# Kernel optimization log

Hardware: AMD Instinct MI355X
Metric: run time of the kernel (lower is better)

Reference implementation:

```python
import jax, jax.numpy as jnp
import numpy as np

D = 1024
H = 16
DH = D // H


def setup_inputs() -> dict:
    key = jax.random.key(0)
    ks = jax.random.split(key, 9)
    s = 1.0 / np.sqrt(D)
    return {
        "x": jax.random.normal(ks[0], (4, 2048, D), dtype=jnp.float32),
        "wq": jax.random.uniform(ks[1], (D, D), jnp.float32, -s, s),
        "bq": jax.random.uniform(ks[2], (D,), jnp.float32, -s, s),
        "wk": jax.random.uniform(ks[3], (D, D), jnp.float32, -s, s),
        "bk": jax.random.uniform(ks[4], (D,), jnp.float32, -s, s),
        "wv": jax.random.uniform(ks[5], (D, D), jnp.float32, -s, s),
        "bv": jax.random.uniform(ks[6], (D,), jnp.float32, -s, s),
        "wo": jax.random.uniform(ks[7], (D, D), jnp.float32, -s, s),
        "bo": jax.random.uniform(ks[8], (D,), jnp.float32, -s, s),
    }


def reference(x, wq, bq, wk, bk, wv, bv, wo, bo):
    B, S, _ = x.shape
    # projections + split heads: [B, S, D] -> [B, H, S, Dh]
    def split(t):
        return t.reshape(B, S, H, DH).transpose(0, 2, 1, 3)
    q = split(x @ wq + bq)
    k = split(x @ wk + bk)
    v = split(x @ wv + bv)
    scale = 1.0 / jnp.sqrt(jnp.float32(DH))
    scores = jnp.einsum("bhqd,bhkd->bhqk", q, k) * scale  # [B,H,S,S]
    att = jax.nn.softmax(scores, axis=-1)
    out = jnp.einsum("bhqk,bhkd->bhqd", att, v)  # [B,H,S,Dh]
    out = out.transpose(0, 2, 1, 3).reshape(B, S, D)
    return out @ wo + bo
```

## Files before the change

kernel.cpp:

```cpp
#include <hip/hip_runtime.h>
#include <stdint.h>

typedef float f32x4 __attribute__((ext_vector_type(4)));
typedef __bf16 bf16x8 __attribute__((ext_vector_type(8)));
typedef unsigned short ushort_t;
typedef ushort_t ushortx8 __attribute__((ext_vector_type(8)));
typedef ushort_t ushortx4 __attribute__((ext_vector_type(4)));

#define DEV static __device__ __forceinline__

DEV ushort_t f2bf(float f) {
  union { float f; uint32_t u; } v; v.f = f;
  uint32_t u = v.u;
  return (ushort_t)((u + 0x7FFFu + ((u >> 16) & 1u)) >> 16);
}

DEV uint32_t pkbf(float a, float b) {
  __bf16 x = (__bf16)a, y = (__bf16)b;
  return (uint32_t)__builtin_bit_cast(unsigned short, x) |
         ((uint32_t)__builtin_bit_cast(unsigned short, y) << 16);
}

DEV void cp16(const void* g, void* l) {
  __builtin_amdgcn_global_load_lds((const __attribute__((address_space(1))) unsigned int*)g,
                                   (__attribute__((address_space(3))) unsigned int*)l,
                                   16, 0, 0);
}

DEV f32x4 mfma16(bf16x8 a, bf16x8 b, f32x4 c) {
  return __builtin_amdgcn_mfma_f32_16x16x32_bf16(a, b, c, 0, 0, 0);
}

__global__ __launch_bounds__(256) void k_prep(
    const float* __restrict__ x, ushort_t* __restrict__ xb,
    const float* __restrict__ wq, const float* __restrict__ wk,
    const float* __restrict__ wv, const float* __restrict__ wo,
    ushort_t* __restrict__ wqkvT, ushort_t* __restrict__ woT) {
  __shared__ float tile[32][33];
  int b = blockIdx.x;
  if (b < 4096) {
    size_t idx = ((size_t)b * 256 + threadIdx.x) * 8;
    const float4* src = (const float4*)(x + idx);
    float4 a = src[0], c = src[1];
    ushortx8 o;
    o[0] = f2bf(a.x); o[1] = f2bf(a.y); o[2] = f2bf(a.z); o[3] = f2bf(a.w);
    o[4] = f2bf(c.x); o[5] = f2bf(c.y); o[6] = f2bf(c.z); o[7] = f2bf(c.w);
    *(ushortx8*)(xb + idx) = o;
  } else {
    int t = b - 4096;
    int which = t >> 10;
    const float* src = (which == 0) ? wq : (which == 1) ? wk : (which == 2) ? wv : wo;
    ushort_t* dst = (which == 0) ? wqkvT
                    : (which == 1) ? wqkvT + 1024 * 1024
                    : (which == 2) ? wqkvT + 2 * 1024 * 1024
                                   : woT;
    int tt = t & 1023;
    int c0 = (tt & 31) * 32, r0 = (tt >> 5) * 32;
    int tx = threadIdx.x & 31, ty = threadIdx.x >> 5;
#pragma unroll
    for (int i = ty; i < 32; i += 8)
      tile[i][tx] = src[(size_t)(r0 + i) * 1024 + c0 + tx];
    __syncthreads();
#pragma unroll
    for (int i = ty; i < 32; i += 8)
      dst[(size_t)(c0 + i) * 1024 + r0 + tx] = f2bf(tile[tx][i]);
  }
}

__global__ __launch_bounds__(256) void k_transpose_v(const ushort_t* __restrict__ vw,
                                                     ushort_t* __restrict__ vtw) {
  __shared__ ushort_t t[64][72];
  int tid = threadIdx.x;
  int bh = blockIdx.y, s0 = blockIdx.x * 64;
#pragma unroll
  for (int n = 0; n < 2; ++n) {
    int row = (tid >> 3) + n * 32, ch = (tid & 7) * 8;
    *(ushortx8*)&t[row][ch] =
        *(const ushortx8*)&vw[((size_t)bh * 2048 + s0 + row) * 64 + ch];
  }
  __syncthreads();
#pragma unroll
  for (int n = 0; n < 2; ++n) {
    int dh = (tid >> 3) + n * 32, sc = (tid & 7) * 8;
    ushortx8 o;
#pragma unroll
    for (int k = 0; k < 8; ++k) o[k] = t[sc + k][dh];
    *(ushortx8*)&vtw[((size_t)bh * 64 + dh) * 2048 + s0 + sc] = o;
  }
}

__global__ __launch_bounds__(512, 2) void k_gemm256(
    const ushort_t* __restrict__ A, const ushort_t* __restrict__ Bt,
    const float* __restrict__ b0, const float* __restrict__ b1,
    const float* __restrict__ b2, ushort_t* __restrict__ qw,
    ushort_t* __restrict__ kw, ushort_t* __restrict__ vw) {
  extern __shared__ ushort_t lds[];
  ushort_t* As = lds;
  ushort_t* Bs = lds + 32768;
  const int K = 1024, NT = 16;
  int tid = threadIdx.x;
  int w = tid >> 6, lane = tid & 63, l16 = lane & 15, lg = lane >> 4;
  int wr = w >> 2, wc = w & 3;
  int m0 = blockIdx.x * 256, n0 = blockIdx.y * 256;

  const ushort_t* Asrc = A + (size_t)(m0 + w * 8 + (lane >> 3)) * K +
                         (size_t)(((lane & 7) ^ (lane >> 3)) * 8);
  const ushort_t* Bsrc = Bt + (size_t)(n0 + w * 8 + (lane >> 3)) * K +
                         (size_t)(((lane & 7) ^ (lane >> 3)) * 8);

  f32x4 acc[8][4] = {};
  bf16x8 a[4][2], b[4][2];
  const int aRow = wr * 128 + l16, bRow = wc * 64 + l16, rsw = l16 & 7;

#pragma unroll
  for (int s = 0; s < 4; ++s)
    cp16(Asrc + (size_t)s * 64 * K, As + s * 4096 + w * 512);
#pragma unroll
  for (int s = 0; s < 4; ++s)
    cp16(Bsrc + (size_t)s * 64 * K, Bs + s * 4096 + w * 512);
  cp16(Asrc + 64, As + 16384 + w * 512);
  cp16(Asrc + (size_t)65536 + 64, As + 16384 + 4096 + w * 512);
  asm volatile("s_waitcnt vmcnt(2)" ::: "memory");
  __builtin_amdgcn_s_barrier();

  for (int t = 0; t < NT; ++t) {
    int cur = t & 1, nxt = cur ^ 1;
    ushort_t* AsC = As + cur * 16384;
    ushort_t* BsC = Bs + cur * 16384;
    ushort_t* AsN = As + nxt * 16384;
    ushort_t* BsN = Bs + nxt * 16384;
    const ushort_t* An = Asrc + (size_t)(t + 1) * 64;
    const ushort_t* Bn = Bsrc + (size_t)(t + 1) * 64;

#pragma unroll
    for (int i2 = 0; i2 < 4; ++i2)
#pragma unroll
      for (int ks = 0; ks < 2; ++ks)
        a[i2][ks] = *(const bf16x8*)&AsC[(aRow + i2 * 16) * 64 +
                                         (((ks << 2) | lg) ^ rsw) * 8];
#pragma unroll
    for (int j2 = 0; j2 < 2; ++j2)
#pragma unroll
      for (int ks = 0; ks < 2; ++ks)
        b[j2][ks] = *(const bf16x8*)&BsC[(bRow + j2 * 16) * 64 +
                                         (((ks << 2) | lg) ^ rsw) * 8];
    cp16(An + (size_t)2 * 65536, AsN + 2 * 4096 + w * 512);
    cp16(An + (size_t)3 * 65536, AsN + 3 * 4096 + w * 512);
    __builtin_amdgcn_s_barrier();
    asm volatile("s_waitcnt lgkmcnt(0)" ::: "memory");
    __builtin_amdgcn_s_setprio(1);
#pragma unroll
    for (int i2 = 0; i2 < 4; ++i2)
#pragma unroll
      for (int j2 = 0; j2 < 2; ++j2)
#pragma unroll
        for (int ks = 0; ks < 2; ++ks)
          acc[i2][j2] = mfma16(a[i2][ks], b[j2][ks], acc[i2][j2]);
    __builtin_amdgcn_s_setprio(0);
    __builtin_amdgcn_s_barrier();

#pragma unroll
    for (int j2 = 2; j2 < 4; ++j2)
#pragma unroll
      for (int ks = 0; ks < 2; ++ks)
        b[j2][ks] = *(const bf16x8*)&BsC[(bRow + j2 * 16) * 64 +
                                         (((ks << 2) | lg) ^ rsw) * 8];
    cp16(Bn, BsN + w * 512);
    cp16(Bn + (size_t)65536, BsN + 4096 + w * 512);
    __builtin_amdgcn_s_barrier();
    asm volatile("s_waitcnt lgkmcnt(0)" ::: "memory");
    __builtin_amdgcn_s_setprio(1);
#pragma unroll
    for (int i2 = 0; i2 < 4; ++i2)
#pragma unroll
      for (int j2 = 2; j2 < 4; ++j2)
#pragma unroll
        for (int ks = 0; ks < 2; ++ks)
          acc[i2][j2] = mfma16(a[i2][ks], b[j2][ks], acc[i2][j2]);
    __builtin_amdgcn_s_setprio(0);
    __builtin_amdgcn_s_barrier();

#pragma unroll
    for (int i2 = 0; i2 < 4; ++i2)
#pragma unroll
      for (int ks = 0; ks < 2; ++ks)
        a[i2][ks] = *(const bf16x8*)&AsC[(aRow + (4 + i2) * 16) * 64 +
                                         (((ks << 2) | lg) ^ rsw) * 8];
    cp16(Bn + (size_t)2 * 65536, BsN + 2 * 4096 + w * 512);
    cp16(Bn + (size_t)3 * 65536, BsN + 3 * 4096 + w * 512);
    __builtin_amdgcn_s_barrier();
    asm volatile("s_waitcnt lgkmcnt(0)" ::: "memory");
    __builtin_amdgcn_s_setprio(1);
#pragma unroll
    for (int i2 = 0; i2 < 4; ++i2)
#pragma unroll
      for (int j2 = 2; j2 < 4; ++j2)
#pragma unroll
        for (int ks = 0; ks < 2; ++ks)
          acc[4 + i2][j2] = mfma16(a[i2][ks], b[j2][ks], acc[4 + i2][j2]);
    __builtin_amdgcn_s_setprio(0);
    __builtin_amdgcn_s_barrier();

    {
      const ushort_t* A2 = Asrc + (size_t)(t + 2) * 64;
      cp16(A2, AsC + w * 512);
      cp16(A2 + (size_t)65536, AsC + 4096 + w * 512);
    }
    asm volatile("s_waitcnt vmcnt(2)" ::: "memory");
    __builtin_amdgcn_s_barrier();
    __builtin_amdgcn_s_setprio(1);
#pragma unroll
    for (int i2 = 0; i2 < 4; ++i2)
#pragma unroll
      for (int j2 = 0; j2 < 2; ++j2)
#pragma unroll
        for (int ks = 0; ks < 2; ++ks)
          acc[4 + i2][j2] = mfma16(a[i2][ks], b[j2][ks], acc[4 + i2][j2]);
    __builtin_amdgcn_s_setprio(0);
    __builtin_amdgcn_s_barrier();
  }

  const float QSCALE = 0.18033688011112042f;
  int p = blockIdx.x >> 2;
  const float* bias = (p == 0) ? b0 : (p == 1) ? b1 : b2;
  ushort_t* dst = (p == 0) ? qw : (p == 1) ? kw : vw;
  float qs = (p == 0) ? QSCALE : 1.0f;
  int cbase = (m0 & 1023) + wr * 128;
#pragma unroll
  for (int i = 0; i < 8; ++i) {
    int oc = cbase + i * 16 + lg * 4;
    int h = oc >> 6, dh0 = oc & 63;
    float4 bb = *(const float4*)&bias[oc];
#pragma unroll
    for (int j = 0; j < 4; ++j) {
      int tok = n0 + wc * 64 + j * 16 + l16;
      size_t base =
          ((size_t)((tok >> 11) * 16 + h) * 2048 + (tok & 2047)) * 64 + dh0;
      ushortx4 pk;
      pk[0] = f2bf((acc[i][j][0] + bb.x) * qs);
      pk[1] = f2bf((acc[i][j][1] + bb.y) * qs);
      pk[2] = f2bf((acc[i][j][2] + bb.z) * qs);
      pk[3] = f2bf((acc[i][j][3] + bb.w) * qs);
      *(ushortx4*)&dst[base] = pk;
    }
  }
}

template <int MODE>
__global__ __launch_bounds__(256, 2) void k_gemm(
    const ushort_t* __restrict__ A, const ushort_t* __restrict__ Bt,
    const float* __restrict__ b0, float* __restrict__ outf) {
  const int K = 1024;
  __shared__ ushort_t As[128 * 32];
  __shared__ ushort_t Bs[128 * 32];
  int tid = threadIdx.x;
  int w = tid >> 6, lane = tid & 63, l16 = lane & 15, lg = lane >> 4;
  int m0 = blockIdx.x * 128, n0 = blockIdx.y * 128;
  int wm = (w >> 1) * 64, wn = (w & 1) * 64;
  f32x4 acc[4][4] = {};

  const ushort_t* Ag = A + (size_t)(m0 + (tid >> 2)) * K + (tid & 3) * 8;
  const ushort_t* Bg = Bt + (size_t)(n0 + (tid >> 2)) * K + (tid & 3) * 8;

  for (int k0 = 0; k0 < K; k0 += 32) {
    cp16(Ag + k0, As + w * 512);
    cp16(Ag + k0 + 64 * K, As + 2048 + w * 512);
    cp16(Bg + k0, Bs + w * 512);
    cp16(Bg + k0 + 64 * K, Bs + 2048 + w * 512);
    __syncthreads();
    bf16x8 af[4], bfr[4];
#pragma unroll
    for (int i = 0; i < 4; ++i)
      af[i] = *(const bf16x8*)&As[(wm + i * 16 + l16) * 32 + lg * 8];
#pragma unroll
    for (int j = 0; j < 4; ++j)
      bfr[j] = *(const bf16x8*)&Bs[(wn + j * 16 + l16) * 32 + lg * 8];
#pragma unroll
    for (int i = 0; i < 4; ++i)
#pragma unroll
      for (int j = 0; j < 4; ++j)
        acc[i][j] = mfma16(af[i], bfr[j], acc[i][j]);
    __syncthreads();
  }

#pragma unroll
  for (int j = 0; j < 4; ++j) {
    int col = n0 + wn + j * 16 + l16;
    float bb = b0[col];
#pragma unroll
    for (int i = 0; i < 4; ++i) {
#pragma unroll
      for (int r = 0; r < 4; ++r) {
        int row = m0 + wm + i * 16 + lg * 4 + r;
        outf[(size_t)row * 1024 + col] = acc[i][j][r] + bb;
      }
    }
  }
}

__global__ __launch_bounds__(512, 4) void k_attn(
    const ushort_t* __restrict__ qg, const ushort_t* __restrict__ kg,
    const ushort_t* __restrict__ vtg, ushort_t* __restrict__ att) {
  __shared__ ushort_t Ks[128 * 64];
  __shared__ ushort_t Vs[64 * 128];
  __shared__ ushort_t Ps[8][16 * 128];
  int tid = threadIdx.x;
  int w = tid >> 6, lane = tid & 63, l16 = lane & 15, lg = lane >> 4;
  int i = blockIdx.x;
  int bh = (i & 7) * 8 + ((i >> 3) & 7);
  int q0 = (i >> 6) * 256;
  const ushort_t* qh = qg + (size_t)bh * 2048 * 64;

  const ushort_t* kstage = kg + (size_t)bh * 2048 * 64 + (size_t)(tid >> 3) * 64 +
                           (size_t)(((tid & 7) ^ ((tid >> 3) & 7)) * 8);
  const ushort_t* vstage = vtg + (size_t)bh * 64 * 2048 + (size_t)(tid >> 4) * 2048 +
                           (size_t)(((tid & 15) ^ ((tid >> 4) & 15)) * 8);

  bf16x8 qf[2][2];
#pragma unroll
  for (int st = 0; st < 2; ++st)
#pragma unroll
    for (int ks = 0; ks < 2; ++ks)
      qf[st][ks] = *(const bf16x8*)(qh + (size_t)(q0 + w * 32 + st * 16 + l16) * 64 +
                                    ks * 32 + lg * 8);

  bf16x8 vone;
#pragma unroll
  for (int t = 0; t < 8; ++t) vone[t] = (__bf16)1.0f;

  f32x4 o[2][5] = {};

  for (int kb = 0; kb < 2048; kb += 128) {
    __syncthreads();
    cp16(kstage + (size_t)kb * 64, Ks + w * 512);
    cp16(kstage + (size_t)(kb + 64) * 64, Ks + 4096 + w * 512);
    cp16(vstage + kb, Vs + w * 512);
    cp16(vstage + kb + (size_t)32 * 2048, Vs + 4096 + w * 512);
    __syncthreads();

#pragma unroll
    for (int hf = 0; hf < 2; ++hf) {
      f32x4 sc[2][4] = {};
#pragma unroll
      for (int jt = 0; jt < 4; ++jt) {
        int row = hf * 64 + jt * 16 + l16;
        bf16x8 kf0 = *(const bf16x8*)&Ks[row * 64 + ((lg) ^ (l16 & 7)) * 8];
        bf16x8 kf1 = *(const bf16x8*)&Ks[row * 64 + ((lg + 4) ^ (l16 & 7)) * 8];
        sc[0][jt] = mfma16(kf0, qf[0][0], sc[0][jt]);
        sc[0][jt] = mfma16(kf1, qf[0][1], sc[0][jt]);
        sc[1][jt] = mfma16(kf0, qf[1][0], sc[1][jt]);
        sc[1][jt] = mfma16(kf1, qf[1][1], sc[1][jt]);
      }
#pragma unroll
      for (int st = 0; st < 2; ++st)
#pragma unroll
        for (int jt = 0; jt < 4; ++jt) {
          float e0 = __builtin_amdgcn_exp2f(sc[st][jt][0]);
          float e1 = __builtin_amdgcn_exp2f(sc[st][jt][1]);
          float e2 = __builtin_amdgcn_exp2f(sc[st][jt][2]);
          float e3 = __builtin_amdgcn_exp2f(sc[st][jt][3]);
          uint32_t* dst =
              (uint32_t*)&Ps[w][l16 * 128 +
                                (((st * 8 + jt * 2 + (lg >> 1)) ^ l16) * 8) +
                                (lg & 1) * 4];
          dst[0] = pkbf(e0, e1);
          dst[1] = pkbf(e2, e3);
        }
#pragma unroll
      for (int ks = 0; ks < 2; ++ks) {
        int kk = hf * 2 + ks;
        bf16x8 pf0 =
            *(const bf16x8*)&Ps[w][l16 * 128 + (((ks * 4 + lg) ^ l16) * 8)];
        bf16x8 pf1 =
            *(const bf16x8*)&Ps[w][l16 * 128 + (((8 + ks * 4 + lg) ^ l16) * 8)];
        o[0][4] = mfma16(pf0, vone, o[0][4]);
        o[1][4] = mfma16(pf1, vone, o[1][4]);
#pragma unroll
        for (int dt = 0; dt < 4; ++dt) {
          int vrow = dt * 16 + l16;
          bf16x8 vf =
              *(const bf16x8*)&Vs[vrow * 128 + (((kk * 4 + lg) ^ l16) * 8)];
          o[0][dt] = mfma16(pf0, vf, o[0][dt]);
          o[1][dt] = mfma16(pf1, vf, o[1][dt]);
        }
      }
    }
  }

  int bi = bh >> 4, h = bh & 15;
#pragma unroll
  for (int st = 0; st < 2; ++st) {
    f32x4 inv;
#pragma unroll
    for (int r = 0; r < 4; ++r) inv[r] = __builtin_amdgcn_rcpf(o[st][4][r]);
#pragma unroll
    for (int dt = 0; dt < 4; ++dt)
#pragma unroll
      for (int r = 0; r < 4; ++r) {
        int srow = q0 + w * 32 + st * 16 + lg * 4 + r;
        int col = h * 64 + dt * 16 + l16;
        att[(size_t)(bi * 2048 + srow) * 1024 + col] = f2bf(o[st][dt][r] * inv[r]);
      }
  }
}

extern "C" void kernel_launch(void* const* d_in, const int* in_sizes, int n_in,
                              void* d_out, int out_size, void* d_ws, size_t ws_size,
                              hipStream_t stream) {
  const float* x = (const float*)d_in[0];
  const float* wq = (const float*)d_in[1];
  const float* bq = (const float*)d_in[2];
  const float* wk = (const float*)d_in[3];
  const float* bk = (const float*)d_in[4];
  const float* wv = (const float*)d_in[5];
  const float* bv = (const float*)d_in[6];
  const float* wo = (const float*)d_in[7];
  const float* bo = (const float*)d_in[8];
  float* out = (float*)d_out;

  char* ws = (char*)d_ws;
  ushort_t* xb = (ushort_t*)(ws);
  ushort_t* wqkvT = (ushort_t*)(ws + 16777216);
  ushort_t* woT = (ushort_t*)(ws + 23068672);
  ushort_t* qw = (ushort_t*)(ws + 25165824);
  ushort_t* kw = (ushort_t*)(ws + 41943040);
  ushort_t* vtw = (ushort_t*)(ws + 58720256);
  ushort_t* att = (ushort_t*)(ws + 75497472);
  ushort_t* vw = att;

  k_prep<<<dim3(8192), dim3(256), 0, stream>>>(x, xb, wq, wk, wv, wo, wqkvT, woT);

  const int GEMM0_LDS = 131072;
  hipFuncSetAttribute(reinterpret_cast<const void*>(&k_gemm256),
                      hipFuncAttributeMaxDynamicSharedMemorySize, GEMM0_LDS);
  k_gemm256<<<dim3(12, 32), dim3(512), GEMM0_LDS, stream>>>(
      wqkvT, xb, bq, bk, bv, qw, kw, vw);

  k_transpose_v<<<dim3(32, 64), dim3(256), 0, stream>>>(vw, vtw);

  k_attn<<<dim3(512), dim3(512), 0, stream>>>(qw, kw, vtw, att);

  k_gemm<1><<<dim3(64, 8), dim3(256), 0, stream>>>(att, woT, bo, out);
}
```

Measured before the change: 276.6 us.

## Halve attention block threads, give each wave 64 query rows for K/V reuse

The attention kernel now runs 256 threads (4 waves) per block instead of 512, and each wave handles 64 query rows (four 16-row subtiles) instead of 32. Each K and V fragment read from LDS now feeds four MFMAs instead of two, which cuts LDS read traffic per flop. Staging is spread across fewer threads, with four copies each for K and V, and the P scratch buffer is widened to match. The cost is higher register use per wave (more accumulators and Q fragments) and fewer waves per block to hide latency.

```diff
diff --git a/kernel.cpp b/kernel.cpp
--- a/kernel.cpp
+++ b/kernel.cpp
@@ -298,12 +298,12 @@
   }
 }
 
-__global__ __launch_bounds__(512, 4) void k_attn(
+__global__ __launch_bounds__(256, 2) void k_attn(
     const ushort_t* __restrict__ qg, const ushort_t* __restrict__ kg,
     const ushort_t* __restrict__ vtg, ushort_t* __restrict__ att) {
   __shared__ ushort_t Ks[128 * 64];
   __shared__ ushort_t Vs[64 * 128];
-  __shared__ ushort_t Ps[8][16 * 128];
+  __shared__ ushort_t Ps[4][16 * 256];
   int tid = threadIdx.x;
   int w = tid >> 6, lane = tid & 63, l16 = lane & 15, lg = lane >> 4;
   int i = blockIdx.x;
@@ -316,72 +316,78 @@
   const ushort_t* vstage = vtg + (size_t)bh * 64 * 2048 + (size_t)(tid >> 4) * 2048 +
                            (size_t)(((tid & 15) ^ ((tid >> 4) & 15)) * 8);
 
-  bf16x8 qf[2][2];
-#pragma unroll
-  for (int st = 0; st < 2; ++st)
+  bf16x8 qf[4][2];
+#pragma unroll
+  for (int st = 0; st < 4; ++st)
 #pragma unroll
     for (int ks = 0; ks < 2; ++ks)
-      qf[st][ks] = *(const bf16x8*)(qh + (size_t)(q0 + w * 32 + st * 16 + l16) * 64 +
+      qf[st][ks] = *(const bf16x8*)(qh + (size_t)(q0 + w * 64 + st * 16 + l16) * 64 +
                                     ks * 32 + lg * 8);
 
   bf16x8 vone;
 #pragma unroll
   for (int t = 0; t < 8; ++t) vone[t] = (__bf16)1.0f;
 
-  f32x4 o[2][5] = {};
+  f32x4 o[4][5] = {};
 
   for (int kb = 0; kb < 2048; kb += 128) {
     __syncthreads();
-    cp16(kstage + (size_t)kb * 64, Ks + w * 512);
-    cp16(kstage + (size_t)(kb + 64) * 64, Ks + 4096 + w * 512);
-    cp16(vstage + kb, Vs + w * 512);
-    cp16(vstage + kb + (size_t)32 * 2048, Vs + 4096 + w * 512);
+#pragma unroll
+    for (int r = 0; r < 4; ++r)
+      cp16(kstage + (size_t)(kb + r * 32) * 64, Ks + r * 2048 + w * 512);
+#pragma unroll
+    for (int r = 0; r < 4; ++r)
+      cp16(vstage + kb + (size_t)(r * 16) * 2048, Vs + r * 2048 + w * 512);
     __syncthreads();
 
 #pragma unroll
     for (int hf = 0; hf < 2; ++hf) {
-      f32x4 sc[2][4] = {};
+      f32x4 sc[4][4] = {};
 #pragma unroll
       for (int jt = 0; jt < 4; ++jt) {
         int row = hf * 64 + jt * 16 + l16;
         bf16x8 kf0 = *(const bf16x8*)&Ks[row * 64 + ((lg) ^ (l16 & 7)) * 8];
         bf16x8 kf1 = *(const bf16x8*)&Ks[row * 64 + ((lg + 4) ^ (l16 & 7)) * 8];
-        sc[0][jt] = mfma16(kf0, qf[0][0], sc[0][jt]);
-        sc[0][jt] = mfma16(kf1, qf[0][1], sc[0][jt]);
-        sc[1][jt] = mfma16(kf0, qf[1][0], sc[1][jt]);
-        sc[1][jt] = mfma16(kf1, qf[1][1], sc[1][jt]);
+#pragma unroll
+        for (int st = 0; st < 4; ++st) {
+          sc[st][jt] = mfma16(kf0, qf[st][0], sc[st][jt]);
+          sc[st][jt] = mfma16(kf1, qf[st][1], sc[st][jt]);
+        }
       }
 #pragma unroll
-      for (int st = 0; st < 2; ++st)
+      for (int st = 0; st < 4; ++st)
 #pragma unroll
         for (int jt = 0; jt < 4; ++jt) {
           float e0 = __builtin_amdgcn_exp2f(sc[st][jt][0]);
           float e1 = __builtin_amdgcn_exp2f(sc[st][jt][1]);
           float e2 = __builtin_amdgcn_exp2f(sc[st][jt][2]);
           float e3 = __builtin_amdgcn_exp2f(sc[st][jt][3]);
-          uint32_t* dst =
-              (uint32_t*)&Ps[w][l16 * 128 +
-                                (((st * 8 + jt * 2 + (lg >> 1)) ^ l16) * 8) +
-                                (lg & 1) * 4];
-          dst[0] = pkbf(e0, e1);
-          dst[1] = pkbf(e2, e3);
+          uint2 pk2;
+          pk2.x = pkbf(e0, e1);
+          pk2.y = pkbf(e2, e3);
+          *(uint2*)&Ps[w][l16 * 256 +
+                          (((st * 8 + jt * 2 + (lg >> 1)) ^ l16) * 8) +
+                          (lg & 1) * 4] = pk2;
         }
 #pragma unroll
       for (int ks = 0; ks < 2; ++ks) {
         int kk = hf * 2 + ks;
-        bf16x8 pf0 =
-            *(const bf16x8*)&Ps[w][l16 * 128 + (((ks * 4 + lg) ^ l16) * 8)];
-        bf16x8 pf1 =
-            *(const bf16x8*)&Ps[w][l16 * 128 + (((8 + ks * 4 + lg) ^ l16) * 8)];
-        o[0][4] = mfma16(pf0, vone, o[0][4]);
-        o[1][4] = mfma16(pf1, vone, o[1][4]);
+        bf16x8 pf[4];
+#pragma unroll
+        for (int st = 0; st < 4; ++st)
+          pf[st] = *(const bf16x8*)&Ps[w][l16 * 256 +
+                                          (((st * 8 + ks * 4 + lg) ^ l16) * 8)];
+#pragma unroll
+        for (int st = 0; st < 4; ++st)
+          o[st][4] = mfma16(pf[st], vone, o[st][4]);
 #pragma unroll
         for (int dt = 0; dt < 4; ++dt) {
           int vrow = dt * 16 + l16;
           bf16x8 vf =
               *(const bf16x8*)&Vs[vrow * 128 + (((kk * 4 + lg) ^ l16) * 8)];
-          o[0][dt] = mfma16(pf0, vf, o[0][dt]);
-          o[1][dt] = mfma16(pf1, vf, o[1][dt]);
+#pragma unroll
+          for (int st = 0; st < 4; ++st)
+            o[st][dt] = mfma16(pf[st], vf, o[st][dt]);
         }
       }
     }
@@ -389,7 +395,7 @@
 
   int bi = bh >> 4, h = bh & 15;
 #pragma unroll
-  for (int st = 0; st < 2; ++st) {
+  for (int st = 0; st < 4; ++st) {
     f32x4 inv;
 #pragma unroll
     for (int r = 0; r < 4; ++r) inv[r] = __builtin_amdgcn_rcpf(o[st][4][r]);
@@ -397,7 +403,7 @@
     for (int dt = 0; dt < 4; ++dt)
 #pragma unroll
       for (int r = 0; r < 4; ++r) {
-        int srow = q0 + w * 32 + st * 16 + lg * 4 + r;
+        int srow = q0 + w * 64 + st * 16 + lg * 4 + r;
         int col = h * 64 + dt * 16 + l16;
         att[(size_t)(bi * 2048 + srow) * 1024 + col] = f2bf(o[st][dt][r] * inv[r]);
       }
@@ -438,7 +444,7 @@
 
   k_transpose_v<<<dim3(32, 64), dim3(256), 0, stream>>>(vw, vtw);
 
-  k_attn<<<dim3(512), dim3(512), 0, stream>>>(qw, kw, vtw, att);
+  k_attn<<<dim3(512), dim3(256), 0, stream>>>(qw, kw, vtw, att);
 
   k_gemm<1><<<dim3(64, 8), dim3(256), 0, stream>>>(att, woT, bo, out);
 }
```

Result: no change. 279.4 us (+1.0%).

## Double-buffer K/V tiles in attention with async prefetch and wave priority

Applied to the files above, without the earlier changes.

The attention loop now walks 64-key tiles with two LDS buffers. It prefetches the next K/V tile while computing on the current one, so each iteration needs one barrier instead of two. Wave priority is raised around the MFMA sections, and the launch-bounds occupancy hint drops from 4 to 2. The last iteration prefetches past the end of the head's K/V data, which can read out of bounds for the final head. Relying on the barrier to order the async LDS loads is a correctness risk.

```diff
diff --git a/kernel.cpp b/kernel.cpp
--- a/kernel.cpp
+++ b/kernel.cpp
@@ -298,11 +298,11 @@
   }
 }
 
-__global__ __launch_bounds__(512, 4) void k_attn(
+__global__ __launch_bounds__(512, 2) void k_attn(
     const ushort_t* __restrict__ qg, const ushort_t* __restrict__ kg,
     const ushort_t* __restrict__ vtg, ushort_t* __restrict__ att) {
-  __shared__ ushort_t Ks[128 * 64];
-  __shared__ ushort_t Vs[64 * 128];
+  __shared__ ushort_t Ks[2][64 * 64];
+  __shared__ ushort_t Vs[2][64 * 64];
   __shared__ ushort_t Ps[8][16 * 128];
   int tid = threadIdx.x;
   int w = tid >> 6, lane = tid & 63, l16 = lane & 15, lg = lane >> 4;
@@ -313,8 +313,8 @@
 
   const ushort_t* kstage = kg + (size_t)bh * 2048 * 64 + (size_t)(tid >> 3) * 64 +
                            (size_t)(((tid & 7) ^ ((tid >> 3) & 7)) * 8);
-  const ushort_t* vstage = vtg + (size_t)bh * 64 * 2048 + (size_t)(tid >> 4) * 2048 +
-                           (size_t)(((tid & 15) ^ ((tid >> 4) & 15)) * 8);
+  const ushort_t* vstage = vtg + (size_t)bh * 64 * 2048 + (size_t)(tid >> 3) * 2048 +
+                           (size_t)(((tid & 7) ^ ((tid >> 3) & 7)) * 8);
 
   bf16x8 qf[2][2];
 #pragma unroll
@@ -330,61 +330,66 @@
 
   f32x4 o[2][5] = {};
 
-  for (int kb = 0; kb < 2048; kb += 128) {
-    __syncthreads();
-    cp16(kstage + (size_t)kb * 64, Ks + w * 512);
-    cp16(kstage + (size_t)(kb + 64) * 64, Ks + 4096 + w * 512);
-    cp16(vstage + kb, Vs + w * 512);
-    cp16(vstage + kb + (size_t)32 * 2048, Vs + 4096 + w * 512);
-    __syncthreads();
-
-#pragma unroll
-    for (int hf = 0; hf < 2; ++hf) {
-      f32x4 sc[2][4] = {};
+  cp16(kstage, &Ks[0][tid * 8]);
+  cp16(vstage, &Vs[0][tid * 8]);
+  __syncthreads();
+
+  for (int t = 0; t < 32; ++t) {
+    int cur = t & 1, nxt = cur ^ 1;
+    cp16(kstage + (size_t)(t + 1) * 64 * 64, &Ks[nxt][tid * 8]);
+    cp16(vstage + (size_t)(t + 1) * 64, &Vs[nxt][tid * 8]);
+
+    f32x4 sc[2][4] = {};
+    __builtin_amdgcn_s_setprio(1);
+#pragma unroll
+    for (int jt = 0; jt < 4; ++jt) {
+      int row = jt * 16 + l16;
+      bf16x8 kf0 = *(const bf16x8*)&Ks[cur][row * 64 + ((lg) ^ (l16 & 7)) * 8];
+      bf16x8 kf1 = *(const bf16x8*)&Ks[cur][row * 64 + ((lg + 4) ^ (l16 & 7)) * 8];
+      sc[0][jt] = mfma16(kf0, qf[0][0], sc[0][jt]);
+      sc[0][jt] = mfma16(kf1, qf[0][1], sc[0][jt]);
+      sc[1][jt] = mfma16(kf0, qf[1][0], sc[1][jt]);
+      sc[1][jt] = mfma16(kf1, qf[1][1], sc[1][jt]);
+    }
+    __builtin_amdgcn_s_setprio(0);
+
+#pragma unroll
+    for (int st = 0; st < 2; ++st)
 #pragma unroll
       for (int jt = 0; jt < 4; ++jt) {
-        int row = hf * 64 + jt * 16 + l16;
-        bf16x8 kf0 = *(const bf16x8*)&Ks[row * 64 + ((lg) ^ (l16 & 7)) * 8];
-        bf16x8 kf1 = *(const bf16x8*)&Ks[row * 64 + ((lg + 4) ^ (l16 & 7)) * 8];
-        sc[0][jt] = mfma16(kf0, qf[0][0], sc[0][jt]);
-        sc[0][jt] = mfma16(kf1, qf[0][1], sc[0][jt]);
-        sc[1][jt] = mfma16(kf0, qf[1][0], sc[1][jt]);
-        sc[1][jt] = mfma16(kf1, qf[1][1], sc[1][jt]);
+        float e0 = __builtin_amdgcn_exp2f(sc[st][jt][0]);
+        float e1 = __builtin_amdgcn_exp2f(sc[st][jt][1]);
+        float e2 = __builtin_amdgcn_exp2f(sc[st][jt][2]);
+        float e3 = __builtin_amdgcn_exp2f(sc[st][jt][3]);
+        uint2 pk2;
+        pk2.x = pkbf(e0, e1);
+        pk2.y = pkbf(e2, e3);
+        *(uint2*)&Ps[w][l16 * 128 +
+                        (((st * 8 + jt * 2 + (lg >> 1)) ^ l16) * 8) +
+                        (lg & 1) * 4] = pk2;
       }
-#pragma unroll
-      for (int st = 0; st < 2; ++st)
-#pragma unroll
-        for (int jt = 0; jt < 4; ++jt) {
-          float e0 = __builtin_amdgcn_exp2f(sc[st][jt][0]);
-          float e1 = __builtin_amdgcn_exp2f(sc[st][jt][1]);
-          float e2 = __builtin_amdgcn_exp2f(sc[st][jt][2]);
-          float e3 = __builtin_amdgcn_exp2f(sc[st][jt][3]);
-          uint32_t* dst =
-              (uint32_t*)&Ps[w][l16 * 128 +
-                                (((st * 8 + jt * 2 + (lg >> 1)) ^ l16) * 8) +
-                                (lg & 1) * 4];
-          dst[0] = pkbf(e0, e1);
-          dst[1] = pkbf(e2, e3);
-        }
-#pragma unroll
-      for (int ks = 0; ks < 2; ++ks) {
-        int kk = hf * 2 + ks;
-        bf16x8 pf0 =
-            *(const bf16x8*)&Ps[w][l16 * 128 + (((ks * 4 + lg) ^ l16) * 8)];
-        bf16x8 pf1 =
-            *(const bf16x8*)&Ps[w][l16 * 128 + (((8 + ks * 4 + lg) ^ l16) * 8)];
-        o[0][4] = mfma16(pf0, vone, o[0][4]);
-        o[1][4] = mfma16(pf1, vone, o[1][4]);
-#pragma unroll
-        for (int dt = 0; dt < 4; ++dt) {
-          int vrow = dt * 16 + l16;
-          bf16x8 vf =
-              *(const bf16x8*)&Vs[vrow * 128 + (((kk * 4 + lg) ^ l16) * 8)];
-          o[0][dt] = mfma16(pf0, vf, o[0][dt]);
-          o[1][dt] = mfma16(pf1, vf, o[1][dt]);
-        }
+
+    __builtin_amdgcn_s_setprio(1);
+#pragma unroll
+    for (int ks = 0; ks < 2; ++ks) {
+      bf16x8 pf0 =
+          *(const bf16x8*)&Ps[w][l16 * 128 + (((ks * 4 + lg) ^ l16) * 8)];
+      bf16x8 pf1 =
+          *(const bf16x8*)&Ps[w][l16 * 128 + (((8 + ks * 4 + lg) ^ l16) * 8)];
+      o[0][4] = mfma16(pf0, vone, o[0][4]);
+      o[1][4] = mfma16(pf1, vone, o[1][4]);
+#pragma unroll
+      for (int dt = 0; dt < 4; ++dt) {
+        int vrow = dt * 16 + l16;
+        bf16x8 vf =
+            *(const bf16x8*)&Vs[cur][vrow * 64 + (((ks * 4 + lg) ^ (l16 & 7)) * 8)];
+        o[0][dt] = mfma16(pf0, vf, o[0][dt]);
+        o[1][dt] = mfma16(pf1, vf, o[1][dt]);
       }
     }
+    __builtin_amdgcn_s_setprio(0);
+
+    __syncthreads();
   }
 
   int bi = bh >> 4, h = bh & 15;
```

Result: no change. 277.5 us (+0.3%).
